# Optimization experiments

Hardware: AMD Instinct MI355X
Metric: run time of the kernel (lower is better)

## Reference

```python
import jax, jax.numpy as jnp
import numpy as np

D_MODEL = 1024
N, L = 4, 2048


def setup_inputs() -> dict:
    key = jax.random.key(0)
    ks = jax.random.split(key, 8)
    s = 0.1
    return {
        "X": jax.random.normal(ks[0], (N, L, D_MODEL), dtype=jnp.float32),
        "W_Q1": jax.random.normal(ks[1], (D_MODEL, D_MODEL), dtype=jnp.float32) * s,
        "W_K1": jax.random.normal(ks[2], (D_MODEL, D_MODEL), dtype=jnp.float32) * s,
        "W_V1": jax.random.normal(ks[3], (D_MODEL, D_MODEL), dtype=jnp.float32) * s,
        "W_Q2": jax.random.normal(ks[4], (D_MODEL, D_MODEL), dtype=jnp.float32) * s,
        "W_K2": jax.random.normal(ks[5], (D_MODEL, D_MODEL), dtype=jnp.float32) * s,
        "W_V2": jax.random.normal(ks[6], (D_MODEL, D_MODEL), dtype=jnp.float32) * s,
        "W_O": jax.random.normal(ks[7], (D_MODEL, 1), dtype=jnp.float32) * s,
        "b_O": jnp.zeros((1, 1), dtype=jnp.float32),
    }


def _attn_block(H, W_Q, W_K, W_V):
    # H: (N, L, D); single-head scaled dot-product attention
    Q = jnp.einsum('nld,dk->nlk', H, W_Q)
    K = jnp.einsum('nld,dk->nlk', H, W_K)
    V = jnp.einsum('nld,dk->nlk', H, W_V)
    scale = jnp.sqrt(jnp.asarray(Q.shape[-1], Q.dtype))
    scores = jnp.einsum('nqd,nkd->nqk', Q, K) / scale  # (N, L, L)
    attn = jax.nn.softmax(scores, axis=-1)
    return jnp.einsum('nqk,nkd->nqd', attn, V)


def reference(X, W_Q1, W_K1, W_V1, W_Q2, W_K2, W_V2, W_O, b_O):
    H1 = _attn_block(X, W_Q1, W_K1, W_V1)
    H2 = _attn_block(H1, W_Q2, W_K2, W_V2)
    pooled = jnp.mean(H2, axis=1)            # (N, D)
    logits = pooled @ W_O + b_O              # (N, 1)
    return jax.nn.sigmoid(logits).squeeze(-1)  # (N,)
```

## Files before the change

kernel.cpp:

```cpp
#include <hip/hip_runtime.h>
#include <hip/hip_bf16.h>
#include <cstdint>


#define DEVFN __device__ __forceinline__

typedef __attribute__((ext_vector_type(8))) short bf16x8;
typedef __attribute__((ext_vector_type(8))) _Float16 f16x8;
typedef __attribute__((ext_vector_type(4))) float f32x4;
typedef unsigned short u16;

DEVFN u16 f2bf(float f) {
    uint32_t x = __float_as_uint(f);
    x += 0x7fffu + ((x >> 16) & 1u);
    return (u16)(x >> 16);
}
DEVFN float bf2f(u16 u) { return __uint_as_float(((uint32_t)u) << 16); }

DEVFN void gload_lds16(const void* g, void* l) {
    __builtin_amdgcn_global_load_lds(
        (const __attribute__((address_space(1))) void*)g,
        (__attribute__((address_space(3))) void*)l, 16, 0, 0);
}

#define MFMA16 __builtin_amdgcn_mfma_f32_16x16x32_bf16

template<int EPI, bool TBUF>
__global__ __launch_bounds__(256, TBUF ? 3 : 4) void gemmk(
    const u16* __restrict__ A, long long aStride,
    const u16* __restrict__ B, long long bStride,
    void* __restrict__ out0, void* __restrict__ out1,
    const float* __restrict__ zrow, long long cStride,
    int M, int N, int K, int lda, int ldb, int ldc, float scale)
{
    constexpr int ASEC  = 128 * 32;
    constexpr int BUFSZ = ASEC + 128 * 32;
    constexpr int NU    = 4;
    constexpr int NB    = TBUF ? 3 : 2;

    __shared__ __align__(16) u16 L[NB * BUFSZ];
    const int tid  = threadIdx.x;
    const int wave = tid >> 6, lane = tid & 63;

    const int gx = gridDim.x, gy = gridDim.y;
    const int nwg = gx * gy * gridDim.z;
    int flat = (blockIdx.z * gy + blockIdx.y) * gx + blockIdx.x;
    flat = (flat & 7) * (nwg >> 3) + (flat >> 3);
    const int bx = flat % gx, by = (flat / gx) % gy, bz = flat / (gx * gy);

    const u16* pA = A + (size_t)bz * aStride;
    const u16* pB = B + (size_t)bz * bStride;
    const int m0 = by * 128, n0 = bx * 128;

    const u16* src[NU];
    int dst[NU];
#pragma unroll
    for (int q = 0; q < 2; q++) {
        const int s = q * 256 + tid, row = s >> 2, c = (s & 3) ^ ((row >> 1) & 3);
        src[q]     = pA + (size_t)(m0 + row) * lda + c * 8;
        dst[q]     = q * 2048 + wave * 512;
        src[2 + q] = pB + (size_t)(n0 + row) * ldb + c * 8;
        dst[2 + q] = ASEC + q * 2048 + wave * 512;
    }

    const int fr = lane & 15, ch = lane >> 4;
    const int wr = (wave >> 1) * 64, wc = (wave & 1) * 64;

    const int NT = K >> 5;
    f32x4 acc[4][4] = {};

    if constexpr (TBUF) {
#pragma unroll
        for (int u = 0; u < NU; u++) { gload_lds16(src[u], &L[dst[u]]); src[u] += 32; }
#pragma unroll
        for (int u = 0; u < NU; u++) { gload_lds16(src[u], &L[BUFSZ + dst[u]]); src[u] += 32; }
        asm volatile("s_waitcnt vmcnt(4)" ::: "memory");
        __builtin_amdgcn_s_barrier();
        __builtin_amdgcn_sched_barrier(0);

        int cIdx = 0, sIdx = 2;
        for (int kt = 0; kt < NT; ++kt) {
            const int cOff = cIdx * BUFSZ;
            if (kt + 2 < NT) {
                const int sOff = sIdx * BUFSZ;
#pragma unroll
                for (int u = 0; u < NU; u++) { gload_lds16(src[u], &L[sOff + dst[u]]); src[u] += 32; }
            }

            bf16x8 ah[4], bh[4];
#pragma unroll
            for (int i = 0; i < 4; i++) {
                const int r = wr + i * 16 + fr;
                ah[i] = *(const bf16x8*)&L[cOff + r * 32 + ((ch ^ ((r >> 1) & 3)) << 3)];
            }
#pragma unroll
            for (int j = 0; j < 4; j++) {
                const int r = wc + j * 16 + fr;
                bh[j] = *(const bf16x8*)&L[cOff + ASEC + r * 32 + ((ch ^ ((r >> 1) & 3)) << 3)];
            }

#pragma unroll
            for (int i = 0; i < 4; i++)
#pragma unroll
                for (int j = 0; j < 4; j++)
                    acc[i][j] = MFMA16(ah[i], bh[j], acc[i][j], 0, 0, 0);

            if (kt + 1 < NT) {
                if (kt + 2 < NT) asm volatile("s_waitcnt vmcnt(4)" ::: "memory");
                else             asm volatile("s_waitcnt vmcnt(0)" ::: "memory");
                __builtin_amdgcn_s_barrier();
                __builtin_amdgcn_sched_barrier(0);
            }
            cIdx = (cIdx == 2) ? 0 : cIdx + 1;
            sIdx = (sIdx == 2) ? 0 : sIdx + 1;
        }
    } else {
#pragma unroll
        for (int u = 0; u < NU; u++) { gload_lds16(src[u], &L[dst[u]]); src[u] += 32; }
        __syncthreads();

        int cur = 0;
        for (int kt = 0; kt < NT; ++kt) {
            const int cOff = cur * BUFSZ;
            const int sOff = BUFSZ - cOff;
            if (kt + 1 < NT) {
#pragma unroll
                for (int u = 0; u < NU; u++) { gload_lds16(src[u], &L[sOff + dst[u]]); src[u] += 32; }
            }

            bf16x8 ah[4], bh[4];
#pragma unroll
            for (int i = 0; i < 4; i++) {
                const int r = wr + i * 16 + fr;
                ah[i] = *(const bf16x8*)&L[cOff + r * 32 + ((ch ^ ((r >> 1) & 3)) << 3)];
            }
#pragma unroll
            for (int j = 0; j < 4; j++) {
                const int r = wc + j * 16 + fr;
                bh[j] = *(const bf16x8*)&L[cOff + ASEC + r * 32 + ((ch ^ ((r >> 1) & 3)) << 3)];
            }

#pragma unroll
            for (int i = 0; i < 4; i++)
#pragma unroll
                for (int j = 0; j < 4; j++)
                    acc[i][j] = MFMA16(ah[i], bh[j], acc[i][j], 0, 0, 0);

            __syncthreads();
            cur ^= 1;
        }
    }

    if constexpr (EPI == 6) {
#pragma unroll
        for (int i = 0; i < 4; i++)
#pragma unroll
            for (int r = 0; r < 4; r++) {
                const int row = m0 + wr + i * 16 + ch * 4 + r;
                const size_t grow = (size_t)bz * 2048 + row;
                float zp = zrow[grow * 32 + 2 * fr] + zrow[grow * 32 + 2 * fr + 1];
                zp += __shfl_xor(zp, 1, 16);
                zp += __shfl_xor(zp, 2, 16);
                zp += __shfl_xor(zp, 4, 16);
                zp += __shfl_xor(zp, 8, 16);
                const float zi = 1.f / zp;
#pragma unroll
                for (int j = 0; j < 4; j++) {
                    const int col = n0 + wc + j * 16 + fr;
                    ((u16*)out0)[(size_t)bz * cStride + (size_t)row * ldc + col] =
                        f2bf(acc[i][j][r] * zi);
                }
            }
    } else {
#pragma unroll
        for (int i = 0; i < 4; i++)
#pragma unroll
            for (int j = 0; j < 4; j++)
#pragma unroll
                for (int r = 0; r < 4; r++) {
                    const int row = m0 + wr + i * 16 + (lane >> 4) * 4 + r;
                    const int col = n0 + wc + j * 16 + (lane & 15);
                    const float v = acc[i][j][r] * scale;
                    if constexpr (EPI == 3) {
                        ((u16*)out0)[(size_t)bz * cStride + (size_t)row * ldc + col] = f2bf(v);
                    } else {
                        ((_Float16*)out0)[(size_t)bz * cStride + (size_t)row * ldc + col] =
                            (_Float16)v;
                    }
                }
    }
}

template<int EPI>
__global__ __launch_bounds__(512, 1) void gemm256(
    const u16* __restrict__ A, long long aStride,
    const u16* __restrict__ B, long long bStride,
    void* __restrict__ out0, void* __restrict__ out1, long long cStride,
    int K, int lda, int ldb, int ldc, float scale)
{
    constexpr int ASEC  = 256 * 32;
    constexpr int BUFSZ = 2 * ASEC;
    constexpr int NU    = 4;

    __shared__ __align__(16) u16 L[3 * BUFSZ];
    const int tid  = threadIdx.x;
    const int wave = tid >> 6, lane = tid & 63;

    const int gx = gridDim.x, gy = gridDim.y;
    const int nwg = gx * gy * gridDim.z;
    int flat = (blockIdx.z * gy + blockIdx.y) * gx + blockIdx.x;
    flat = (flat & 7) * (nwg >> 3) + (flat >> 3);
    const int bx = flat % gx, by = (flat / gx) % gy, bz = flat / (gx * gy);

    const u16* pA = A + (size_t)bz * aStride;
    const u16* pB = B + (size_t)bz * bStride;
    const int m0 = by * 256, n0 = bx * 256;

    const u16* src[NU];
    int dst[NU];
#pragma unroll
    for (int q = 0; q < 2; q++) {
        const int s = q * 512 + tid, row = s >> 2, c = (s & 3) ^ ((row >> 1) & 3);
        src[q]     = pA + (size_t)(m0 + row) * lda + c * 8;
        dst[q]     = q * 4096 + wave * 512;
        src[2 + q] = pB + (size_t)(n0 + row) * ldb + c * 8;
        dst[2 + q] = ASEC + q * 4096 + wave * 512;
    }

    const int fr = lane & 15, ch = lane >> 4;
    const int wm = (wave >> 2) * 128;
    const int wn = (wave & 3) * 64;

    const int NT = K >> 5;

#pragma unroll
    for (int u = 0; u < NU; u++) { gload_lds16(src[u], &L[dst[u]]); src[u] += 32; }
#pragma unroll
    for (int u = 0; u < NU; u++) { gload_lds16(src[u], &L[BUFSZ + dst[u]]); src[u] += 32; }
    asm volatile("s_waitcnt vmcnt(4)" ::: "memory");
    __builtin_amdgcn_s_barrier();
    __builtin_amdgcn_sched_barrier(0);

    f32x4 acc[8][4] = {};
    int cIdx = 0, sIdx = 2;

    for (int kt = 0; kt < NT; ++kt) {
        const int cOff = cIdx * BUFSZ;
        if (kt + 2 < NT) {
            const int sOff = sIdx * BUFSZ;
#pragma unroll
            for (int u = 0; u < NU; u++) { gload_lds16(src[u], &L[sOff + dst[u]]); src[u] += 32; }
        }

        bf16x8 ah[8], bh[4];
#pragma unroll
        for (int i = 0; i < 8; i++) {
            const int r = wm + i * 16 + fr;
            ah[i] = *(const bf16x8*)&L[cOff + r * 32 + ((ch ^ ((r >> 1) & 3)) << 3)];
        }
#pragma unroll
        for (int j = 0; j < 4; j++) {
            const int r = wn + j * 16 + fr;
            bh[j] = *(const bf16x8*)&L[cOff + ASEC + r * 32 + ((ch ^ ((r >> 1) & 3)) << 3)];
        }

#pragma unroll
        for (int i = 0; i < 8; i++)
#pragma unroll
            for (int j = 0; j < 4; j++)
                acc[i][j] = MFMA16(ah[i], bh[j], acc[i][j], 0, 0, 0);

        if (kt + 1 < NT) {
            if (kt + 2 < NT) asm volatile("s_waitcnt vmcnt(4)" ::: "memory");
            else             asm volatile("s_waitcnt vmcnt(0)" ::: "memory");
            __builtin_amdgcn_s_barrier();
            __builtin_amdgcn_sched_barrier(0);
        }
        cIdx = (cIdx == 2) ? 0 : cIdx + 1;
        sIdx = (sIdx == 2) ? 0 : sIdx + 1;
    }

    if constexpr (EPI == 5) {
#pragma unroll
        for (int i = 0; i < 8; i++)
#pragma unroll
            for (int r = 0; r < 4; r++) {
                const int rowb = m0 + wm + i * 16 + ch * 4 + r;
                float s = 0.f;
#pragma unroll
                for (int j = 0; j < 4; j++) {
                    const int col = n0 + wn + j * 16 + fr;
                    const float e = __expf(acc[i][j][r] * scale - 60.f);
                    s += e;
                    ((u16*)out0)[(size_t)bz * cStride + (size_t)rowb * ldc + col] = f2bf(e);
                }
                s += __shfl_xor(s, 1, 16);
                s += __shfl_xor(s, 2, 16);
                s += __shfl_xor(s, 4, 16);
                s += __shfl_xor(s, 8, 16);
                if (fr == 0)
                    ((float*)out1)[((size_t)bz * 2048 + rowb) * 32 + ((n0 + wn) >> 6)] = s;
            }
    } else {
#pragma unroll
        for (int i = 0; i < 8; i++)
#pragma unroll
            for (int j = 0; j < 4; j++)
#pragma unroll
                for (int r = 0; r < 4; r++) {
                    const int row = m0 + wm + i * 16 + ch * 4 + r;
                    const int col = n0 + wn + j * 16 + fr;
                    ((_Float16*)out0)[(size_t)bz * cStride + (size_t)row * ldc + col] =
                        (_Float16)(acc[i][j][r] * scale);
                }
    }
}

__global__ __launch_bounds__(512, 1) void gemm_tv256(
    const u16* __restrict__ Xb, const u16* __restrict__ Mt1,
    const u16* __restrict__ Wv1T, u16* __restrict__ Tb, u16* __restrict__ Vtb)
{
    constexpr int ASEC  = 256 * 32;
    constexpr int BUFSZ = 2 * ASEC;
    constexpr int NU    = 4;

    __shared__ __align__(16) u16 L[3 * BUFSZ];
    const int tid  = threadIdx.x;
    const int wave = tid >> 6, lane = tid & 63;

    const int x = blockIdx.x & 7;
    const int l = blockIdx.x >> 3;
    const int op = l & 1, u = l >> 1;
    const u16* pA;
    const u16* pB;
    u16* outp;
    int m0, n0, ldc;
    if (op == 0) {
        pA = Xb;  pB = Mt1;  outp = Tb;  ldc = 1024;
        m0 = (x * 4 + (u >> 2)) * 256;  n0 = (u & 3) * 256;
    } else {
        pA = Wv1T; pB = Xb;  outp = Vtb; ldc = 8192;
        m0 = (u & 3) * 256;  n0 = (x * 4 + (u >> 2)) * 256;
    }

    const u16* src[NU];
    int dst[NU];
#pragma unroll
    for (int q = 0; q < 2; q++) {
        const int s = q * 512 + tid, row = s >> 2, c = (s & 3) ^ ((row >> 1) & 3);
        src[q]     = pA + (size_t)(m0 + row) * 1024 + c * 8;
        dst[q]     = q * 4096 + wave * 512;
        src[2 + q] = pB + (size_t)(n0 + row) * 1024 + c * 8;
        dst[2 + q] = ASEC + q * 4096 + wave * 512;
    }

    const int fr = lane & 15, ch = lane >> 4;
    const int wm = (wave >> 2) * 128;
    const int wn = (wave & 3) * 64;

#pragma unroll
    for (int q = 0; q < NU; q++) { gload_lds16(src[q], &L[dst[q]]); src[q] += 32; }
#pragma unroll
    for (int q = 0; q < NU; q++) { gload_lds16(src[q], &L[BUFSZ + dst[q]]); src[q] += 32; }
    asm volatile("s_waitcnt vmcnt(4)" ::: "memory");
    __builtin_amdgcn_s_barrier();
    __builtin_amdgcn_sched_barrier(0);

    f32x4 acc[8][4] = {};
    int cIdx = 0, sIdx = 2;

    for (int kt = 0; kt < 32; ++kt) {
        const int cOff = cIdx * BUFSZ;
        if (kt + 2 < 32) {
            const int sOff = sIdx * BUFSZ;
#pragma unroll
            for (int q = 0; q < NU; q++) { gload_lds16(src[q], &L[sOff + dst[q]]); src[q] += 32; }
        }

        bf16x8 ah[8], bh[4];
#pragma unroll
        for (int i = 0; i < 8; i++) {
            const int r = wm + i * 16 + fr;
            ah[i] = *(const bf16x8*)&L[cOff + r * 32 + ((ch ^ ((r >> 1) & 3)) << 3)];
        }
#pragma unroll
        for (int j = 0; j < 4; j++) {
            const int r = wn + j * 16 + fr;
            bh[j] = *(const bf16x8*)&L[cOff + ASEC + r * 32 + ((ch ^ ((r >> 1) & 3)) << 3)];
        }

#pragma unroll
        for (int i = 0; i < 8; i++)
#pragma unroll
            for (int j = 0; j < 4; j++)
                acc[i][j] = MFMA16(ah[i], bh[j], acc[i][j], 0, 0, 0);

        if (kt + 1 < 32) {
            if (kt + 2 < 32) asm volatile("s_waitcnt vmcnt(4)" ::: "memory");
            else             asm volatile("s_waitcnt vmcnt(0)" ::: "memory");
            __builtin_amdgcn_s_barrier();
            __builtin_amdgcn_sched_barrier(0);
        }
        cIdx = (cIdx == 2) ? 0 : cIdx + 1;
        sIdx = (sIdx == 2) ? 0 : sIdx + 1;
    }

#pragma unroll
    for (int i = 0; i < 8; i++)
#pragma unroll
        for (int j = 0; j < 4; j++)
#pragma unroll
            for (int r = 0; r < 4; r++) {
                const int row = m0 + wm + i * 16 + ch * 4 + r;
                const int col = n0 + wn + j * 16 + fr;
                outp[(size_t)row * ldc + col] = f2bf(acc[i][j][r]);
            }
}

__global__ __launch_bounds__(256) void prep_all(
    const float* __restrict__ X,
    const float* __restrict__ W0, const float* __restrict__ W1,
    const float* __restrict__ W2, const float* __restrict__ W3,
    const float* __restrict__ Wv1, const float* __restrict__ Wv2,
    const float* __restrict__ wO,
    u16* __restrict__ Xb, u16* __restrict__ Wcat,
    u16* __restrict__ Wv1T, float* __restrict__ wv)
{
    const int blk = blockIdx.x, tid = threadIdx.x;
    __shared__ float t[64][65];

    if (blk < 8192) {
        const size_t i = ((size_t)blk * 256 + tid) * 4;
        const float4 v = *(const float4*)&X[i];
        ushort4 h;
        h.x = f2bf(v.x); h.y = f2bf(v.y); h.z = f2bf(v.z); h.w = f2bf(v.w);
        *(ushort4*)&Xb[i] = h;
    } else if (blk < 12288) {
        const int w = (blk - 8192) >> 10, ib = (blk - 8192) & 1023;
        const float* W = (w == 0) ? W0 : (w == 1) ? W1 : (w == 2) ? W2 : W3;
        u16* o = Wcat + (size_t)w * 1048576;
        const size_t i = ((size_t)ib * 256 + tid) * 4;
        const float4 v = *(const float4*)&W[i];
        ushort4 h;
        h.x = f2bf(v.x); h.y = f2bf(v.y); h.z = f2bf(v.z); h.w = f2bf(v.w);
        *(ushort4*)&o[i] = h;
    } else if (blk < 12544) {
        const int tb = blk - 12288;
        const int r0 = (tb >> 4) * 64, c0 = (tb & 15) * 64;
#pragma unroll
        for (int it = 0; it < 16; it++) {
            const int idx = it * 256 + tid, rr = idx >> 6, cc = idx & 63;
            t[rr][cc] = Wv1[(size_t)(r0 + rr) * 1024 + (c0 + cc)];
        }
        __syncthreads();
#pragma unroll
        for (int it = 0; it < 16; it++) {
            const int idx = it * 256 + tid, nn = idx >> 6, kk = idx & 63;
            Wv1T[(size_t)(c0 + nn) * 1024 + (r0 + kk)] = f2bf(t[kk][nn]);
        }
    } else {
        const int d = (blk - 12544) * 16 + (tid >> 4);
        const int lx = tid & 15;
        const float* row = Wv2 + (size_t)d * 1024;
        float s = 0.f;
#pragma unroll
        for (int it = 0; it < 16; it++) {
            const int j = it * 64 + lx * 4;
            const float4 a = *(const float4*)&row[j];
            const float4 w = *(const float4*)&wO[j];
            s += a.x * w.x + a.y * w.y + a.z * w.z + a.w * w.w;
        }
#pragma unroll
        for (int o = 8; o; o >>= 1) s += __shfl_xor(s, o, 16);
        if (lx == 0) wv[d] = s;
    }
}

__global__ __launch_bounds__(256) void mid_head(
    const _Float16* __restrict__ S, float* __restrict__ part,
    const u16* __restrict__ H1, const float* __restrict__ wv,
    float* __restrict__ u)
{
    const int blk = blockIdx.x, tid = threadIdx.x;
    __shared__ float redm[4], reds[4];

    if (blk < 512) {
        const int b = blk >> 7, chunk = blk & 127;
        const _Float16* Sb = S + (size_t)b * (2048 * 2048) + (size_t)chunk * 16 * 2048;
        float acc[8] = {};

        for (int r = 0; r < 16; r++) {
            const _Float16* row = Sb + (size_t)r * 2048;
            const f16x8 hv = *(const f16x8*)&row[tid * 8];
            float v[8];
#pragma unroll
            for (int j = 0; j < 8; j++) v[j] = (float)hv[j];

            float m = v[0];
#pragma unroll
            for (int j = 1; j < 8; j++) m = fmaxf(m, v[j]);
            for (int o = 32; o; o >>= 1) m = fmaxf(m, __shfl_xor(m, o));
            if ((tid & 63) == 0) redm[tid >> 6] = m;
            __syncthreads();
            m = fmaxf(fmaxf(redm[0], redm[1]), fmaxf(redm[2], redm[3]));

            float e[8], s = 0.f;
#pragma unroll
            for (int j = 0; j < 8; j++) { e[j] = __expf(v[j] - m); s += e[j]; }
            for (int o = 32; o; o >>= 1) s += __shfl_xor(s, o);
            if ((tid & 63) == 0) reds[tid >> 6] = s;
            __syncthreads();
            const float inv = 1.f / (reds[0] + reds[1] + reds[2] + reds[3]);
#pragma unroll
            for (int j = 0; j < 8; j++) acc[j] += e[j] * inv;
            __syncthreads();
        }

        float* p = part + ((size_t)(b * 128 + chunk)) * 2048;
#pragma unroll
        for (int j = 0; j < 8; j++) p[tid * 8 + j] = acc[j];
    } else {
        const int r = (blk - 512) * 16 + (tid >> 4);
        const int lx = tid & 15;
        const u16* row = H1 + (size_t)r * 1024;
        float s = 0.f;
#pragma unroll
        for (int it = 0; it < 8; it++) {
            const int d = it * 128 + lx * 8;
            const bf16x8 h = *(const bf16x8*)&row[d];
#pragma unroll
            for (int j = 0; j < 8; j++) s += bf2f((u16)h[j]) * wv[d + j];
        }
#pragma unroll
        for (int o = 8; o; o >>= 1) s += __shfl_xor(s, o, 16);
        if (lx == 0) u[r] = s;
    }
}

__global__ __launch_bounds__(256) void tail2(
    const float* __restrict__ part, const float* __restrict__ u,
    float* __restrict__ partial)
{
    const int blk = blockIdx.x, tid = threadIdx.x;
    const int b = blk >> 5;
    const int kl = tid & 63;
    const int k = (blk & 31) * 64 + kl;
    const int cg = tid >> 6;
    float s = 0.f;
#pragma unroll 4
    for (int c = 0; c < 32; c++)
        s += part[((size_t)(b * 128 + cg * 32 + c)) * 2048 + k];
    __shared__ float red[4][64];
    red[cg][kl] = s;
    __syncthreads();
    if (cg == 0) {
        float v = (red[0][kl] + red[1][kl] + red[2][kl] + red[3][kl])
                  * u[b * 2048 + k];
        for (int o = 32; o; o >>= 1) v += __shfl_xor(v, o);
        if (kl == 0) partial[blk] = v;
    }
}

__global__ void head_final(const float* __restrict__ partial,
                           const float* __restrict__ bO, float* __restrict__ out)
{
    const int t = threadIdx.x;
    float v = partial[t];
#pragma unroll
    for (int o = 16; o; o >>= 1) v += __shfl_xor(v, o);
    if ((t & 31) == 0) {
        const float logit = v * (1.f / 2048.f) + bO[0];
        out[t >> 5] = 1.f / (1.f + __expf(-logit));
    }
}

extern "C" void kernel_launch(void* const* d_in, const int* in_sizes, int n_in,
                              void* d_out, int out_size, void* d_ws, size_t ws_size,
                              hipStream_t stream)
{
    const float* X   = (const float*)d_in[0];
    const float* Wq1 = (const float*)d_in[1];
    const float* Wk1 = (const float*)d_in[2];
    const float* Wv1 = (const float*)d_in[3];
    const float* Wq2 = (const float*)d_in[4];
    const float* Wk2 = (const float*)d_in[5];
    const float* Wv2 = (const float*)d_in[6];
    const float* WO  = (const float*)d_in[7];
    const float* bO  = (const float*)d_in[8];
    float* out = (float*)d_out;

    uint8_t* ws = (uint8_t*)d_ws;
    const size_t MB = 1ull << 20;
    u16* Xb   = (u16*)(ws + 0);
    u16* Tb   = (u16*)(ws + 32 * MB);
    float* part    = (float*)(ws + 80 * MB);
    float* partial = (float*)(ws + 85 * MB);
    float* wv      = (float*)(ws + 86 * MB);
    float* ud      = (float*)(ws + 87 * MB);
    float* Zpart   = (float*)(ws + 88 * MB);
    u16* Vtb  = (u16*)(ws + 96 * MB);
    u16* Wcat = (u16*)(ws + 128 * MB);
    u16* Eb   = (u16*)(ws + 152 * MB);
    _Float16* Sh = (_Float16*)(ws + 152 * MB);

    auto Wslot = [&](int i) { return Wcat + (size_t)i * 1048576; };

    prep_all<<<12608, 256, 0, stream>>>(
        X, Wq1, Wq2, Wk1, Wk2, Wv1, Wv2, WO, Xb, Wcat, Wslot(5), wv);
    gemmk<3, true><<<dim3(8, 8, 2), 256, 0, stream>>>(
        Wslot(2), 1048576, Wslot(0), 1048576, Wslot(4), nullptr, nullptr,
        2 * 1048576LL, 1024, 1024, 1024, 1024, 1024, 1024, 1.f);

    const long long LD2 = 2048LL * 1024;
    const long long EST = 2048LL * 2048;

    gemm_tv256<<<256, 512, 0, stream>>>(Xb, Wslot(4), Wslot(5), Tb, Vtb);
    gemm256<5><<<dim3(8, 8, 4), 512, 0, stream>>>(
        Tb, LD2, Xb, LD2, Eb, Zpart, EST,
        1024, 1024, 1024, 2048, 0.03125f);
    gemmk<6, true><<<dim3(8, 16, 4), 256, 0, stream>>>(
        Eb, EST, Vtb, 2048, Xb, nullptr, Zpart, LD2,
        2048, 1024, 2048, 2048, 8192, 1024, 1.f);

    gemmk<3, true><<<dim3(8, 64, 1), 256, 0, stream>>>(
        Xb, 0, Wslot(6), 0, Tb, nullptr, nullptr, 0,
        8192, 1024, 1024, 1024, 1024, 1024, 1.f);
    gemm256<8><<<dim3(8, 8, 4), 512, 0, stream>>>(
        Tb, LD2, Xb, LD2, Sh, nullptr, EST,
        1024, 1024, 1024, 2048, 0.03125f);

    mid_head<<<1024, 256, 0, stream>>>(Sh, part, Xb, wv, ud);
    tail2<<<128, 256, 0, stream>>>(part, ud, partial);
    head_final<<<1, 128, 0, stream>>>(partial, bO, out);
}
```

Baseline: 239.2 us.

## Add 256x128-tile triple-buffered GEMM for PV and second projection

Introduces a new gemm_tall kernel with 256x128 output tiles per 256-thread workgroup (each wave computing 128x64), a three-stage LDS ring with direct global-to-LDS loads and explicit vmcnt waits. The PV product (with softmax row normalisation epilogue) and the X·W projection GEMM now use it instead of the 128x128 gemmk kernel. The aim is more MFMA work per LDS fragment load and fewer barriers per tile. The cost is higher register pressure (32 accumulators per thread) and fewer workgroups, which may hurt occupancy or load balance. The diff also appears to add a stray bf16 epilogue onto the tail of the preceding kernel.

```diff
diff --git a/kernel.cpp b/kernel.cpp
--- a/kernel.cpp
+++ b/kernel.cpp
@@ -151,12 +151,118 @@
         }
     }
 
+#pragma unroll
+    for (int i = 0; i < 4; i++)
+#pragma unroll
+        for (int j = 0; j < 4; j++)
+#pragma unroll
+            for (int r = 0; r < 4; r++) {
+                const int row = m0 + wr + i * 16 + (lane >> 4) * 4 + r;
+                const int col = n0 + wc + j * 16 + (lane & 15);
+                ((u16*)out0)[(size_t)bz * cStride + (size_t)row * ldc + col] =
+                    f2bf(acc[i][j][r] * scale);
+            }
+}
+
+template<int EPI>
+__global__ __launch_bounds__(256, 2) void gemm_tall(
+    const u16* __restrict__ A, long long aStride,
+    const u16* __restrict__ B, long long bStride,
+    void* __restrict__ out0, const float* __restrict__ zrow, long long cStride,
+    int K, int lda, int ldb, int ldc, float scale)
+{
+    constexpr int ASEC  = 256 * 32;
+    constexpr int BUFSZ = ASEC + 128 * 32;
+    constexpr int NU    = 6;
+
+    __shared__ __align__(16) u16 L[3 * BUFSZ];
+    const int tid  = threadIdx.x;
+    const int wave = tid >> 6, lane = tid & 63;
+
+    const int gx = gridDim.x, gy = gridDim.y;
+    const int nwg = gx * gy * gridDim.z;
+    int flat = (blockIdx.z * gy + blockIdx.y) * gx + blockIdx.x;
+    flat = (flat & 7) * (nwg >> 3) + (flat >> 3);
+    const int bx = flat % gx, by = (flat / gx) % gy, bz = flat / (gx * gy);
+
+    const u16* pA = A + (size_t)bz * aStride;
+    const u16* pB = B + (size_t)bz * bStride;
+    const int m0 = by * 256, n0 = bx * 128;
+
+    const u16* src[NU];
+    int dst[NU];
+#pragma unroll
+    for (int q = 0; q < 4; q++) {
+        const int s = q * 256 + tid, row = s >> 2, c = (s & 3) ^ ((row >> 1) & 3);
+        src[q] = pA + (size_t)(m0 + row) * lda + c * 8;
+        dst[q] = q * 2048 + wave * 512;
+    }
+#pragma unroll
+    for (int q = 0; q < 2; q++) {
+        const int s = q * 256 + tid, row = s >> 2, c = (s & 3) ^ ((row >> 1) & 3);
+        src[4 + q] = pB + (size_t)(n0 + row) * ldb + c * 8;
+        dst[4 + q] = ASEC + q * 2048 + wave * 512;
+    }
+
+    const int fr = lane & 15, ch = lane >> 4;
+    const int wm = (wave >> 1) * 128;
+    const int wn = (wave & 1) * 64;
+
+    const int NT = K >> 5;
+
+#pragma unroll
+    for (int u = 0; u < NU; u++) { gload_lds16(src[u], &L[dst[u]]); src[u] += 32; }
+#pragma unroll
+    for (int u = 0; u < NU; u++) { gload_lds16(src[u], &L[BUFSZ + dst[u]]); src[u] += 32; }
+    asm volatile("s_waitcnt vmcnt(6)" ::: "memory");
+    __builtin_amdgcn_s_barrier();
+    __builtin_amdgcn_sched_barrier(0);
+
+    f32x4 acc[8][4] = {};
+    int cIdx = 0, sIdx = 2;
+
+    for (int kt = 0; kt < NT; ++kt) {
+        const int cOff = cIdx * BUFSZ;
+        if (kt + 2 < NT) {
+            const int sOff = sIdx * BUFSZ;
+#pragma unroll
+            for (int u = 0; u < NU; u++) { gload_lds16(src[u], &L[sOff + dst[u]]); src[u] += 32; }
+        }
+
+        bf16x8 ah[8], bh[4];
+#pragma unroll
+        for (int i = 0; i < 8; i++) {
+            const int r = wm + i * 16 + fr;
+            ah[i] = *(const bf16x8*)&L[cOff + r * 32 + ((ch ^ ((r >> 1) & 3)) << 3)];
+        }
+#pragma unroll
+        for (int j = 0; j < 4; j++) {
+            const int r = wn + j * 16 + fr;
+            bh[j] = *(const bf16x8*)&L[cOff + ASEC + r * 32 + ((ch ^ ((r >> 1) & 3)) << 3)];
+        }
+
+#pragma unroll
+        for (int i = 0; i < 8; i++)
+#pragma unroll
+            for (int j = 0; j < 4; j++)
+                acc[i][j] = MFMA16(ah[i], bh[j], acc[i][j], 0, 0, 0);
+
+        if (kt + 1 < NT) {
+            if (kt + 2 < NT) asm volatile("s_waitcnt vmcnt(6)" ::: "memory");
+            else             asm volatile("s_waitcnt vmcnt(0)" ::: "memory");
+            __builtin_amdgcn_s_barrier();
+            __builtin_amdgcn_sched_barrier(0);
+        }
+        cIdx = (cIdx == 2) ? 0 : cIdx + 1;
+        sIdx = (sIdx == 2) ? 0 : sIdx + 1;
+    }
+
     if constexpr (EPI == 6) {
 #pragma unroll
-        for (int i = 0; i < 4; i++)
+        for (int i = 0; i < 8; i++)
 #pragma unroll
             for (int r = 0; r < 4; r++) {
-                const int row = m0 + wr + i * 16 + ch * 4 + r;
+                const int row = m0 + wm + i * 16 + ch * 4 + r;
                 const size_t grow = (size_t)bz * 2048 + row;
                 float zp = zrow[grow * 32 + 2 * fr] + zrow[grow * 32 + 2 * fr + 1];
                 zp += __shfl_xor(zp, 1, 16);
@@ -166,27 +272,22 @@
                 const float zi = 1.f / zp;
 #pragma unroll
                 for (int j = 0; j < 4; j++) {
-                    const int col = n0 + wc + j * 16 + fr;
+                    const int col = n0 + wn + j * 16 + fr;
                     ((u16*)out0)[(size_t)bz * cStride + (size_t)row * ldc + col] =
                         f2bf(acc[i][j][r] * zi);
                 }
             }
     } else {
 #pragma unroll
-        for (int i = 0; i < 4; i++)
+        for (int i = 0; i < 8; i++)
 #pragma unroll
             for (int j = 0; j < 4; j++)
 #pragma unroll
                 for (int r = 0; r < 4; r++) {
-                    const int row = m0 + wr + i * 16 + (lane >> 4) * 4 + r;
-                    const int col = n0 + wc + j * 16 + (lane & 15);
-                    const float v = acc[i][j][r] * scale;
-                    if constexpr (EPI == 3) {
-                        ((u16*)out0)[(size_t)bz * cStride + (size_t)row * ldc + col] = f2bf(v);
-                    } else {
-                        ((_Float16*)out0)[(size_t)bz * cStride + (size_t)row * ldc + col] =
-                            (_Float16)v;
-                    }
+                    const int row = m0 + wm + i * 16 + ch * 4 + r;
+                    const int col = n0 + wn + j * 16 + fr;
+                    ((u16*)out0)[(size_t)bz * cStride + (size_t)row * ldc + col] =
+                        f2bf(acc[i][j][r] * scale);
                 }
     }
 }
@@ -618,13 +719,13 @@
     gemm256<5><<<dim3(8, 8, 4), 512, 0, stream>>>(
         Tb, LD2, Xb, LD2, Eb, Zpart, EST,
         1024, 1024, 1024, 2048, 0.03125f);
-    gemmk<6, true><<<dim3(8, 16, 4), 256, 0, stream>>>(
-        Eb, EST, Vtb, 2048, Xb, nullptr, Zpart, LD2,
-        2048, 1024, 2048, 2048, 8192, 1024, 1.f);
-
-    gemmk<3, true><<<dim3(8, 64, 1), 256, 0, stream>>>(
-        Xb, 0, Wslot(6), 0, Tb, nullptr, nullptr, 0,
-        8192, 1024, 1024, 1024, 1024, 1024, 1.f);
+    gemm_tall<6><<<dim3(8, 8, 4), 256, 0, stream>>>(
+        Eb, EST, Vtb, 2048, Xb, Zpart, LD2,
+        2048, 2048, 8192, 1024, 1.f);
+
+    gemm_tall<3><<<dim3(8, 32, 1), 256, 0, stream>>>(
+        Xb, 0, Wslot(6), 0, Tb, nullptr, 0,
+        1024, 1024, 1024, 1024, 1.f);
     gemm256<8><<<dim3(8, 8, 4), 512, 0, stream>>>(
         Tb, LD2, Xb, LD2, Sh, nullptr, EST,
         1024, 1024, 1024, 2048, 0.03125f);
```

After: 242.9 us. Within noise of the previous version (+1.5%).
